# Optimization experiments

Hardware: AMD Instinct MI355X
Metric: run time of the kernel (lower is better)

The kernel has to match this reference:

```python
import jax, jax.numpy as jnp
import numpy as np

EPS = 1e-5
SELECT_NUM = 10   # hard-coded in Support_AUG_Image
NEIGHBOR_K = 3
SEMI_K = 3


def _conv(x, w):
    return jax.lax.conv_general_dilated(x, w, (1, 1), 'SAME',
                                        dimension_numbers=('NCHW', 'OIHW', 'NCHW'))


def _bn(x, g, b):
    # BatchNorm2d, training mode: biased batch stats over (N, H, W)
    mu = jnp.mean(x, (0, 2, 3), keepdims=True)
    var = jnp.mean((x - mu) ** 2, (0, 2, 3), keepdims=True)
    return g[None, :, None, None] * (x - mu) * jax.lax.rsqrt(var + EPS) + b[None, :, None, None]


def _lrelu(x):
    return jnp.where(x >= 0, x, 0.2 * x)


def _pool(x):
    return jax.lax.reduce_window(x, -jnp.inf, jax.lax.max,
                                 (1, 1, 2, 2), (1, 1, 2, 2), 'VALID')


def _features(x, params):
    # conv-bn-lrelu-pool, conv-bn-lrelu-pool, conv-bn-lrelu, conv-bn-lrelu
    for i, (w, g, b) in enumerate(params):
        x = _lrelu(_bn(_conv(x, w), g, b))
        if i < 2:
            x = _pool(x)
    return x  # [N, 64, 21, 21] for 84x84 input


def _descriptors(feat):
    # [B, C, h, w] -> [B, h*w, C], rows L2-normalized (query local descriptors)
    B, C = feat.shape[0], feat.shape[1]
    d = feat.reshape(B, C, -1).transpose(0, 2, 1)
    return d / jnp.sqrt(jnp.sum(d * d, -1, keepdims=True))


def _col_normalize(s):
    # [C, m]: L2-normalize each column (support descriptor)
    return s / jnp.sqrt(jnp.sum(s * s, 0, keepdims=True))


def _img2class_sim(q_desc, S, k):
    # q_desc [B, n, C] row-normalized; S [K, C, m] raw support banks.
    # Per class (K small, fixed): cosine sims [B, n, m], top-k over m, sum.
    sims = []
    for j in range(S.shape[0]):
        inner = q_desc @ _col_normalize(S[j])          # [B, n, m]
        tv = jax.lax.top_k(inner, k)[0]                # [B, n, k]
        sims.append(jnp.sum(tv, axis=(1, 2)))
    return jnp.stack(sims, 1)                          # [B, K]


def _forward(input1, input2, input3, params):
    K, shot = input2.shape[0], input2.shape[1]
    q = _features(input1, params)                      # [Bq, 64, 21, 21]
    sup = _features(input2.reshape((-1,) + input2.shape[2:]), params)
    C, h, w = sup.shape[1], sup.shape[2], sup.shape[3]
    # per class: permute(1,0,2,3).view(C,-1) -> [K, C, shot*h*w]
    S = sup.reshape(K, shot, C, h, w).transpose(0, 2, 1, 3, 4).reshape(K, C, shot * h * w)
    u = _features(input3, params)                      # [Bu, 64, 21, 21]

    # Support_AUG_Image: similarity of unlabeled pool vs support, softmax over classes,
    # then append top-10 unlabeled feature maps (raw) to each class bank.
    u_desc = _descriptors(u)
    sim_u = jax.nn.softmax(_img2class_sim(u_desc, S, SEMI_K), axis=1)  # [Bu, K]
    aug = []
    for j in range(K):
        idx = jax.lax.top_k(sim_u[:, j], SELECT_NUM)[1]                # [10]
        sel = u[idx].transpose(1, 0, 2, 3).reshape(C, -1)              # [C, 10*h*w]
        aug.append(jnp.concatenate([S[j], sel], axis=1))
    S_aug = jnp.stack(aug, 0)                          # [K, C, shot*h*w + 10*h*w]

    # ImgtoClass_Metric on queries vs augmented support
    q_desc = _descriptors(q)
    return _img2class_sim(q_desc, S_aug, NEIGHBOR_K)   # [Bq, K]


def setup_inputs() -> dict:
    key = jax.random.key(0)
    ks = jax.random.split(key, 8)
    inp = {
        'input1': jax.random.normal(ks[0], (75, 3, 84, 84), jnp.float32),
        'input2': jax.random.normal(ks[1], (5, 5, 3, 84, 84), jnp.float32),
        'input3': jax.random.normal(ks[2], (64, 3, 84, 84), jnp.float32),
        'w1': jax.random.normal(ks[3], (64, 3, 3, 3), jnp.float32) * 0.1,
        'w2': jax.random.normal(ks[4], (64, 64, 3, 3), jnp.float32) * 0.05,
        'w3': jax.random.normal(ks[5], (64, 64, 3, 3), jnp.float32) * 0.05,
        'w4': jax.random.normal(ks[6], (64, 64, 3, 3), jnp.float32) * 0.05,
    }
    for i in (1, 2, 3, 4):
        inp[f'g{i}'] = jnp.ones((64,), jnp.float32)
        inp[f'b{i}'] = jnp.zeros((64,), jnp.float32)
    return inp


def reference(input1, input2, input3, w1, g1, b1, w2, g2, b2, w3, g3, b3, w4, g4, b4):
    params = [(w1, g1, b1), (w2, g2, b2), (w3, g3, b3), (w4, g4, b4)]
    return _forward(input1, input2, input3, params)
```

## Files before the change

### kernel.cpp

```cpp
#include <hip/hip_runtime.h>
#include <hip/hip_bf16.h>
#include <math.h>

typedef __hip_bfloat16 bf16;
typedef __attribute__((ext_vector_type(8))) short short8;
typedef __attribute__((ext_vector_type(4))) float floatx4;
typedef __attribute__((ext_vector_type(4))) unsigned short ushort4v;

#define LRELU(v) ((v) < 0.f ? 0.2f * (v) : (v))

__device__ __forceinline__ float b2f(bf16 x) { return __bfloat162float(x); }
__device__ __forceinline__ int img_group(int n) { return n < 75 ? 0 : (n < 100 ? 1 : 2); }

__global__ __launch_bounds__(64) void detect_kernel(
    const void* in1, const void* in2, const void* in3,
    const void* w1, const void* w2, const void* w3, const void* w4,
    const void* g1, const void* g2, const void* g3, const void* g4,
    int* __restrict__ flags)
{
  int t = threadIdx.x;
  if (t >= 11) return;
  const void* p = nullptr; int nh = 384, isg = 0;
  switch (t) {
    case 0: p = in1; break;  case 1: p = in2; break;  case 2: p = in3; break;
    case 3: p = w1;  break;  case 4: p = w2;  break;  case 5: p = w3;  break;
    case 6: p = w4;  break;
    case 7: p = g1; nh = 64; isg = 1; break;
    case 8: p = g2; nh = 64; isg = 1; break;
    case 9: p = g3; nh = 64; isg = 1; break;
    case 10: p = g4; nh = 64; isg = 1; break;
  }
  const unsigned short* h = (const unsigned short*)p;
  int cnt = 0;
  for (int i = 0; i < nh; ++i) {
    unsigned short v = h[i];
    if (isg) {
      if (v == 0) ++cnt;
    } else {
      int e = (v >> 7) & 0xFF;
      if (e >= 160 || (e > 0 && e <= 80)) ++cnt;
    }
  }
  flags[t] = isg ? (cnt >= 16) : (cnt >= 48);
}

#define ZT0 167280
#define ZT1 1972592
#define ZT2 2896240
#define ZT3 3819888
#define ZT4 4565104
__device__ __forceinline__ void border_yx(int b, int W, int* y, int* x) {
  if (b < W) { *y = 0; *x = b; }
  else if (b < 2 * W) { *y = W - 1; *x = b - W; }
  else { int cc = b - 2 * W; *y = 1 + (cc >> 1); *x = (cc & 1) ? (W - 1) : 0; }
}
__global__ __launch_bounds__(256) void zero_pads(
    bf16* __restrict__ imgp, bf16* __restrict__ p1t,
    bf16* __restrict__ p2t, bf16* __restrict__ f3t, bf16* __restrict__ descAll)
{
  int i = blockIdx.x * 256 + threadIdx.x;
  bf16 z = __float2bfloat16(0.f);
  if (i < ZT0) {
    int plane = i / 340, b = i % 340;
    int y, x; border_yx(b, 86, &y, &x);
    imgp[((size_t)plane * 86 + y) * 86 + x] = z;
  } else if (i < ZT1) {
    int r = i - ZT0;
    int img = r / (172 * 64); r %= 172 * 64;
    int colb = r >> 6, ch = r & 63;
    int y, x; border_yx(colb, 44, &y, &x);
    p1t[(((size_t)img * 1936) + y * 44 + x) * 64 + ch] = z;
  } else if (i < ZT2) {
    int r = i - ZT1;
    int img = r / (88 * 64); r %= 88 * 64;
    int colb = r >> 6, ch = r & 63;
    int y, x; border_yx(colb, 23, &y, &x);
    p2t[(((size_t)img * 529) + y * 23 + x) * 64 + ch] = z;
  } else if (i < ZT3) {
    int r = i - ZT2;
    int img = r / (88 * 64); r %= 88 * 64;
    int colb = r >> 6, ch = r & 63;
    int y, x; border_yx(colb, 23, &y, &x);
    f3t[(((size_t)img * 529) + y * 23 + x) * 64 + ch] = z;
  } else if (i < ZT4) {
    int r = i - ZT3;
    int img = r / (71 * 64); r %= 71 * 64;
    int row = 441 + (r >> 6), ch = r & 63;
    descAll[((size_t)img * 512 + row) * 64 + ch] = z;
  }
}

#define NIMG 3471552
#define BIMG 13562
#define NWP  110592
#define BWP  432
#define BW1  8
#define BGB  2
#define NPART (4 * 164 * 128)
#define NZ (NPART + 320 + 375)
#define BZ  331
__global__ __launch_bounds__(256) void setup_all(
    const void* in1, const void* in2, const void* in3,
    const void* w1, const void* w2, const void* w3, const void* w4,
    const void* g1, const void* b1, const void* g2, const void* b2,
    const void* g3, const void* b3, const void* g4, const void* b4,
    const int* __restrict__ flags,
    bf16* __restrict__ imgp, bf16* __restrict__ w1p,
    bf16* __restrict__ wp2, bf16* __restrict__ wp3, bf16* __restrict__ wp4,
    float* __restrict__ gb, float* __restrict__ part,
    float* __restrict__ uscore, float* __restrict__ qscore)
{
  int b = blockIdx.x;
  if (b < BIMG) {
    int k = b * 256 + threadIdx.x;
    if (k >= NIMG) return;
    const void* src; int idx, f;
    if (k < 75 * 21168)       { src = in1; idx = k;               f = flags[0]; }
    else if (k < 100 * 21168) { src = in2; idx = k - 75 * 21168;  f = flags[1]; }
    else                      { src = in3; idx = k - 100 * 21168; f = flags[2]; }
    bf16 v = f ? __float2bfloat16(((const float*)src)[idx]) : ((const bf16*)src)[idx];
    int n = k / 21168, r = k % 21168;
    int ci = r / 7056, pix = r % 7056;
    int y = pix / 84, x = pix % 84;
    imgp[((size_t)(n * 3 + ci) * 86 + y + 1) * 86 + x + 1] = v;
  } else if (b < BIMG + BWP) {
    int idx = (b - BIMG) * 256 + threadIdx.x;
    if (idx >= NWP) return;
    int which = idx / 36864, i = idx % 36864;
    const void* src = which == 0 ? w2 : (which == 1 ? w3 : w4);
    bf16* dst = which == 0 ? wp2 : (which == 1 ? wp3 : wp4);
    int f = flags[4 + which];
    float v = f ? ((const float*)src)[i] : b2f(((const bf16*)src)[i]);
    int co = i / 576, ci = (i / 9) % 64, tap = i % 9;
    dst[((size_t)tap * 64 + co) * 64 + ci] = __float2bfloat16(v);
  } else if (b < BIMG + BWP + BW1) {
    int i = (b - BIMG - BWP) * 256 + threadIdx.x;
    if (i >= 2048) return;
    int co = i >> 5, k = i & 31;
    float v = 0.f;
    if (k < 27) {
      int f = flags[3];
      v = f ? ((const float*)w1)[co * 27 + k] : b2f(((const bf16*)w1)[co * 27 + k]);
    }
    w1p[i] = __float2bfloat16(v);
  } else if (b < BIMG + BWP + BW1 + BGB) {
    int i = (b - BIMG - BWP - BW1) * 256 + threadIdx.x;
    if (i >= 512) return;
    int which = i >> 6, cc = i & 63;
    const void* s;
    switch (which) {
      case 0: s = g1; break; case 1: s = b1; break;
      case 2: s = g2; break; case 3: s = b2; break;
      case 4: s = g3; break; case 5: s = b3; break;
      case 6: s = g4; break; default: s = b4; break;
    }
    int isg = !(which & 1);
    int f = isg ? flags[7 + (which >> 1)] : 0;
    gb[i] = f ? ((const float*)s)[cc] : b2f(((const bf16*)s)[cc]);
  } else {
    int i = (b - BIMG - BWP - BW1 - BGB) * 256 + threadIdx.x;
    if (i < NPART) part[i] = 0.f;
    else if (i < NPART + 320) uscore[i - NPART] = 0.f;
    else if (i < NZ) qscore[i - NPART - 320] = 0.f;
  }
}

__global__ __launch_bounds__(256) void conv1_stats_mfma(
    const bf16* __restrict__ imgp, const bf16* __restrict__ w1p,
    float* __restrict__ part)
{
  __shared__ float sacc[128];
  int n = blockIdx.x, tile = blockIdx.y;
  int lane = threadIdx.x & 63;
  int q = lane >> 4, c = lane & 15;
  int wave = threadIdx.x >> 6;
  int p = tile * 64 + wave * 16 + c;
  bool valid = p < 7056;
  int pc = valid ? p : 0;
  int y = pc / 84, x = pc % 84;
  const short* ib = (const short*)(imgp + (size_t)n * 3 * 86 * 86);
  short bs[8];
  #pragma unroll
  for (int j = 0; j < 8; ++j) {
    int k = q * 8 + j;
    int ci = k / 9, tap = k - ci * 9;
    int dy = tap / 3, dx = tap - dy * 3;
    bs[j] = (k < 27 && valid) ? ib[(ci * 86 + y + dy) * 86 + x + dx] : (short)0;
  }
  short8 B = {bs[0], bs[1], bs[2], bs[3], bs[4], bs[5], bs[6], bs[7]};
  float s[16], sq[16];
  #pragma unroll
  for (int t = 0; t < 4; ++t) {
    const short* ap = (const short*)w1p + (t * 16 + c) * 32 + q * 8;
    short8 A = *(const short8*)ap;
    floatx4 acc = {0.f, 0.f, 0.f, 0.f};
    acc = __builtin_amdgcn_mfma_f32_16x16x32_bf16(A, B, acc, 0, 0, 0);
    #pragma unroll
    for (int r = 0; r < 4; ++r) { s[t * 4 + r] = acc[r]; sq[t * 4 + r] = acc[r] * acc[r]; }
  }
  #pragma unroll
  for (int off = 1; off < 16; off <<= 1)
    #pragma unroll
    for (int i = 0; i < 16; ++i) {
      s[i]  += __shfl_xor(s[i], off);
      sq[i] += __shfl_xor(sq[i], off);
    }
  if (threadIdx.x < 128) sacc[threadIdx.x] = 0.f;
  __syncthreads();
  if (c == 0) {
    #pragma unroll
    for (int t = 0; t < 4; ++t)
      #pragma unroll
      for (int r = 0; r < 4; ++r) {
        int co = t * 16 + q * 4 + r;
        atomicAdd(&sacc[co], s[t * 4 + r]);
        atomicAdd(&sacc[64 + co], sq[t * 4 + r]);
      }
  }
  __syncthreads();
  if (threadIdx.x < 128) atomicAdd(&part[n * 128 + threadIdx.x], sacc[threadIdx.x]);
}

__global__ __launch_bounds__(256) void finalize_kernel(
    const float* __restrict__ part, const float* __restrict__ gam, const float* __restrict__ bet,
    float* __restrict__ scl, float* __restrict__ sht, float HWf)
{
  int t = threadIdx.x;
  if (t >= 192) return;
  int g = t / 64, c = t % 64;
  const int starts[3] = {0, 75, 100}, cnts[3] = {75, 25, 64};
  float S = 0.f, Q = 0.f;
  for (int im = starts[g]; im < starts[g] + cnts[g]; ++im) {
    S += part[im * 128 + c];
    Q += part[im * 128 + 64 + c];
  }
  float N = (float)cnts[g] * HWf;
  float mean = S / N;
  float var = fmaxf(Q / N - mean * mean, 0.f);
  float rstd = rsqrtf(var + 1e-5f);
  float sc = gam[c] * rstd;
  scl[t] = sc;
  sht[t] = bet[c] - mean * sc;
}

__global__ __launch_bounds__(256) void conv1_pool_mfma(
    const bf16* __restrict__ imgp, const bf16* __restrict__ w1p,
    const float* __restrict__ scl, const float* __restrict__ sht,
    bf16* __restrict__ p1t)
{
  int n = blockIdx.x, tile = blockIdx.y;
  int lane = threadIdx.x & 63, wave = threadIdx.x >> 6;
  int q = lane >> 4, c = lane & 15;
  int pp = tile * 64 + wave * 16 + c;
  bool valid = pp < 1764;
  int pc = valid ? pp : 0;
  int py = pc / 42, px = pc % 42;
  int g = img_group(n);
  const short* ib = (const short*)(imgp + (size_t)n * 3 * 86 * 86);
  short8 B[4];
  #pragma unroll
  for (int quad = 0; quad < 4; ++quad) {
    int y = 2 * py + (quad >> 1), x = 2 * px + (quad & 1);
    short bs[8];
    #pragma unroll
    for (int j = 0; j < 8; ++j) {
      int k = q * 8 + j;
      int ci = k / 9, tap = k - ci * 9;
      int dy = tap / 3, dx = tap - dy * 3;
      bs[j] = (k < 27) ? ib[(ci * 86 + y + dy) * 86 + x + dx] : (short)0;
    }
    B[quad] = (short8){bs[0], bs[1], bs[2], bs[3], bs[4], bs[5], bs[6], bs[7]};
  }
  bf16* ob = p1t + ((size_t)n * 1936 + (py + 1) * 44 + px + 1) * 64;
  #pragma unroll
  for (int t = 0; t < 4; ++t) {
    const short* ap = (const short*)w1p + (t * 16 + c) * 32 + q * 8;
    short8 A = *(const short8*)ap;
    floatx4 a0 = {0.f,0.f,0.f,0.f}, a1 = a0, a2 = a0, a3 = a0;
    a0 = __builtin_amdgcn_mfma_f32_16x16x32_bf16(A, B[0], a0, 0, 0, 0);
    a1 = __builtin_amdgcn_mfma_f32_16x16x32_bf16(A, B[1], a1, 0, 0, 0);
    a2 = __builtin_amdgcn_mfma_f32_16x16x32_bf16(A, B[2], a2, 0, 0, 0);
    a3 = __builtin_amdgcn_mfma_f32_16x16x32_bf16(A, B[3], a3, 0, 0, 0);
    if (valid) {
      ushort4v st;
      #pragma unroll
      for (int r = 0; r < 4; ++r) {
        int co = t * 16 + q * 4 + r;
        float sc_ = scl[g * 64 + co], sh_ = sht[g * 64 + co];
        float v0 = a0[r] * sc_ + sh_; v0 = LRELU(v0);
        float v1 = a1[r] * sc_ + sh_; v1 = LRELU(v1);
        float v2 = a2[r] * sc_ + sh_; v2 = LRELU(v2);
        float v3 = a3[r] * sc_ + sh_; v3 = LRELU(v3);
        float best = fmaxf(fmaxf(v0, v1), fmaxf(v2, v3));
        bf16 bv = __float2bfloat16(best);
        st[r] = *(unsigned short*)&bv;
      }
      *(ushort4v*)(ob + t * 16 + q * 4) = st;
    }
  }
}

__global__ __launch_bounds__(256) void bnt_kernel(
    const float* __restrict__ in, const float* __restrict__ scl, const float* __restrict__ sht,
    bf16* __restrict__ outp, int HW, int W, int PW, int PHPW)
{
  __shared__ bf16 tile[64][65];
  int n = blockIdx.x, t0 = blockIdx.y * 64;
  int g = img_group(n);
  for (int idx = threadIdx.x; idx < 4096; idx += 256) {
    int ci = idx >> 6, pix = idx & 63;
    int p = t0 + pix;
    float v = 0.f;
    if (p < HW) {
      v = in[((size_t)n * 64 + ci) * HW + p] * scl[g * 64 + ci] + sht[g * 64 + ci];
      v = LRELU(v);
    }
    tile[pix][ci] = __float2bfloat16(v);
  }
  __syncthreads();
  for (int idx = threadIdx.x; idx < 4096; idx += 256) {
    int pix = idx >> 6, ci = idx & 63;
    int p = t0 + pix;
    if (p < HW) {
      int y = p / W, x = p % W;
      outp[((size_t)n * PHPW + (y + 1) * PW + (x + 1)) * 64 + ci] = tile[pix][ci];
    }
  }
}

__global__ __launch_bounds__(256) void conv_mfma_kernel(
    const bf16* __restrict__ in_t, const bf16* __restrict__ wp,
    void* __restrict__ outp, int HW, int W, int PW, int PHPW, int out_is_f32,
    float* __restrict__ part)
{
  __shared__ float sacc[128];
  if (threadIdx.x < 128) sacc[threadIdx.x] = 0.f;
  __syncthreads();
  int n = blockIdx.x, tile = blockIdx.y;
  int wave = threadIdx.x >> 6, lane = threadIdx.x & 63;
  int q = lane >> 4, c = lane & 15;
  int p = tile * 64 + wave * 16 + c;
  bool valid = p < HW;
  int pc = valid ? p : HW - 1;
  int y = pc / W, x = pc % W;
  const bf16* ibase = in_t + ((size_t)n * PHPW + y * PW + x) * 64;

  short8 B0[9], B1[9];
  #pragma unroll
  for (int dy = 0; dy < 3; ++dy)
    #pragma unroll
    for (int dx = 0; dx < 3; ++dx) {
      const short* bp = (const short*)(ibase + (dy * PW + dx) * 64) + q * 8;
      B0[dy * 3 + dx] = *(const short8*)bp;
      B1[dy * 3 + dx] = *(const short8*)(bp + 32);
    }

  for (int t = 0; t < 4; ++t) {
    floatx4 acc = {0.f, 0.f, 0.f, 0.f};
    #pragma unroll
    for (int tap = 0; tap < 9; ++tap) {
      const short* ap = (const short*)(wp + ((size_t)tap * 64 + t * 16 + c) * 64) + q * 8;
      short8 A0 = *(const short8*)ap;
      short8 A1 = *(const short8*)(ap + 32);
      acc = __builtin_amdgcn_mfma_f32_16x16x32_bf16(A0, B0[tap], acc, 0, 0, 0);
      acc = __builtin_amdgcn_mfma_f32_16x16x32_bf16(A1, B1[tap], acc, 0, 0, 0);
    }
    float sv[4], qv[4];
    #pragma unroll
    for (int r = 0; r < 4; ++r) {
      float v = valid ? acc[r] : 0.f;
      sv[r] = v; qv[r] = v * v;
    }
    #pragma unroll
    for (int off = 1; off < 16; off <<= 1)
      #pragma unroll
      for (int r = 0; r < 4; ++r) {
        sv[r] += __shfl_xor(sv[r], off);
        qv[r] += __shfl_xor(qv[r], off);
      }
    if (c == 0) {
      #pragma unroll
      for (int r = 0; r < 4; ++r) {
        int co = t * 16 + q * 4 + r;
        atomicAdd(&sacc[co], sv[r]);
        atomicAdd(&sacc[64 + co], qv[r]);
      }
    }
    if (valid) {
      #pragma unroll
      for (int r = 0; r < 4; ++r) {
        int co = t * 16 + q * 4 + r;
        size_t oidx = ((size_t)n * 64 + co) * HW + p;
        if (out_is_f32) ((float*)outp)[oidx] = acc[r];
        else ((bf16*)outp)[oidx] = __float2bfloat16(acc[r]);
      }
    }
  }
  __syncthreads();
  if (threadIdx.x < 128) atomicAdd(&part[n * 128 + threadIdx.x], sacc[threadIdx.x]);
}

__global__ __launch_bounds__(256) void bn2_pool_t(
    const bf16* __restrict__ c2, const float* __restrict__ scl, const float* __restrict__ sht,
    bf16* __restrict__ p2t)
{
  __shared__ bf16 tile[64][65];
  int n = blockIdx.x, t0 = blockIdx.y * 64;
  int g = img_group(n);
  for (int idx = threadIdx.x; idx < 4096; idx += 256) {
    int co = idx >> 6, pix = idx & 63;
    int p = t0 + pix;
    bf16 outv = __float2bfloat16(0.f);
    if (p < 441) {
      float sc = scl[g * 64 + co], sh = sht[g * 64 + co];
      int py = p / 21, px = p % 21;
      const bf16* base = c2 + ((size_t)n * 64 + co) * 1764;
      float best = -1e30f;
      #pragma unroll
      for (int dy = 0; dy < 2; ++dy)
        #pragma unroll
        for (int dx = 0; dx < 2; ++dx) {
          float v = b2f(base[(2 * py + dy) * 42 + 2 * px + dx]) * sc + sh;
          v = LRELU(v);
          best = fmaxf(best, v);
        }
      outv = __float2bfloat16(best);
    }
    tile[pix][co] = outv;
  }
  __syncthreads();
  for (int idx = threadIdx.x; idx < 4096; idx += 256) {
    int pix = idx >> 6, co = idx & 63;
    int p = t0 + pix;
    if (p < 441) {
      int y = p / 21, x = p % 21;
      p2t[((size_t)n * 529 + (y + 1) * 23 + x + 1) * 64 + co] = tile[pix][co];
    }
  }
}

__global__ __launch_bounds__(256) void bn_norm_desc(
    const float* __restrict__ feat, const float* __restrict__ scl, const float* __restrict__ sht,
    bf16* __restrict__ descAll)
{
  __shared__ float tile[64][65];
  int n = blockIdx.x, t0 = blockIdx.y * 64;
  int g = img_group(n);
  for (int idx = threadIdx.x; idx < 4096; idx += 256) {
    int ci = idx >> 6, pix = idx & 63;
    int p = t0 + pix;
    float v = 0.f;
    if (p < 441) {
      v = feat[((size_t)n * 64 + ci) * 441 + p] * scl[g * 64 + ci] + sht[g * 64 + ci];
      v = LRELU(v);
    }
    tile[pix][ci] = v;
  }
  __syncthreads();
  int pix = threadIdx.x >> 2, quar = threadIdx.x & 3;
  float ss = 0.f;
  #pragma unroll
  for (int c = 0; c < 16; ++c) { float v = tile[pix][quar * 16 + c]; ss += v * v; }
  ss += __shfl_xor(ss, 1);
  ss += __shfl_xor(ss, 2);
  int p = t0 + pix;
  float inv = (p < 441) ? rsqrtf(ss) : 0.f;
  bf16* o = descAll + ((size_t)n * 512 + p) * 64 + quar * 16;
  #pragma unroll
  for (int c = 0; c < 16; ++c) o[c] = __float2bfloat16(tile[pix][quar * 16 + c] * inv);
}

__global__ __launch_bounds__(256) void sbank_copy(
    const bf16* __restrict__ descAll, bf16* __restrict__ SnT)
{
  int j = blockIdx.x / 9, chunk = blockIdx.x % 9;
  int col = chunk * 256 + threadIdx.x;
  short* o = (short*)(SnT + ((size_t)j * 2304 + col) * 64);
  if (col < 2205) {
    int shot = col / 441, pos = col % 441;
    const short* s = (const short*)(descAll + ((size_t)(75 + j * 5 + shot) * 512 + pos) * 64);
    #pragma unroll
    for (int k = 0; k < 8; ++k) *(short8*)(o + k * 8) = *(const short8*)(s + k * 8);
  } else {
    short8 z = {0,0,0,0,0,0,0,0};
    #pragma unroll
    for (int k = 0; k < 8; ++k) *(short8*)(o + k * 8) = z;
  }
}

__global__ __launch_bounds__(256) void saug_copy(
    const bf16* __restrict__ descAll, const bf16* __restrict__ SnT,
    const int* __restrict__ sel, bf16* __restrict__ SaT)
{
  int j = blockIdx.x / 26, chunk = blockIdx.x % 26;
  int col = chunk * 256 + threadIdx.x;
  short* o = (short*)(SaT + ((size_t)j * 6656 + col) * 64);
  const short* s;
  if (col < 2205) {
    s = (const short*)(SnT + ((size_t)j * 2304 + col) * 64);
  } else if (col < 6615) {
    int rel = col - 2205;
    int i = rel / 441, pos = rel % 441;
    int img = 100 + sel[j * 10 + i];
    s = (const short*)(descAll + ((size_t)img * 512 + pos) * 64);
  } else {
    short8 z = {0,0,0,0,0,0,0,0};
    #pragma unroll
    for (int k = 0; k < 8; ++k) *(short8*)(o + k * 8) = z;
    return;
  }
  #pragma unroll
  for (int k = 0; k < 8; ++k) *(short8*)(o + k * 8) = *(const short8*)(s + k * 8);
}

#define SIM_NS 4
__global__ __launch_bounds__(448) void sim_mfma_kernel(
    const bf16* __restrict__ desc, const bf16* __restrict__ bankT,
    float* __restrict__ partial, int m, int mp)
{
  __shared__ short lds[2][64 * 72];
  int img = blockIdx.x, cls = blockIdx.y, slice = blockIdx.z;
  int tid = threadIdx.x;
  int wave = tid >> 6, lane = tid & 63;
  int q = lane >> 4, c = lane & 15;
  int R = wave * 64;

  const short* dp = (const short*)(desc + ((size_t)img * 512 + R + c) * 64) + q * 8;
  short8 b0l = *(const short8*)dp;          short8 b0h = *(const short8*)(dp + 32);
  short8 b1l = *(const short8*)(dp + 1024); short8 b1h = *(const short8*)(dp + 1056);
  short8 b2l = *(const short8*)(dp + 2048); short8 b2h = *(const short8*)(dp + 2080);
  short8 b3l = *(const short8*)(dp + 3072); short8 b3h = *(const short8*)(dp + 3104);

  float t0[4], t1[4], t2[4];
  #pragma unroll
  for (int i = 0; i < 4; ++i) { t0[i] = -1e4f; t1[i] = -1e4f; t2[i] = -1e4f; }

  const floatx4 z4 = {0.f, 0.f, 0.f, 0.f};

  const short* bankc = (const short*)(bankT + (size_t)cls * mp * 64);
  int nc = (mp >> 6) / SIM_NS;
  int ch0 = slice * nc, ch1 = ch0 + nc;
  int nfull = m >> 4;

  for (int s = tid; s < 512; s += 448) {
    int col = s >> 3, part = s & 7;
    *(short8*)(&lds[0][col * 72 + part * 8]) =
        *(const short8*)(bankc + ((size_t)ch0 * 64 + col) * 64 + part * 8);
  }
  __syncthreads();

  for (int ch = ch0; ch < ch1; ++ch) {
    int cur = (ch - ch0) & 1;
    if (ch + 1 < ch1) {
      const short* src = bankc + (size_t)(ch + 1) * 4096;
      for (int s = tid; s < 512; s += 448) {
        int col = s >> 3, part = s & 7;
        *(short8*)(&lds[cur ^ 1][col * 72 + part * 8]) = *(const short8*)(src + (size_t)col * 64 + part * 8);
      }
    }
    #pragma unroll
    for (int t = 0; t < 4; ++t) {
      const short* lp = &lds[cur][(t * 16 + c) * 72 + q * 8];
      short8 A0 = *(const short8*)lp;
      short8 A1 = *(const short8*)(lp + 32);
      floatx4 a0 = __builtin_amdgcn_mfma_f32_16x16x32_bf16(A0, b0l, z4, 0, 0, 0);
      floatx4 a1 = __builtin_amdgcn_mfma_f32_16x16x32_bf16(A0, b1l, z4, 0, 0, 0);
      floatx4 a2 = __builtin_amdgcn_mfma_f32_16x16x32_bf16(A0, b2l, z4, 0, 0, 0);
      floatx4 a3 = __builtin_amdgcn_mfma_f32_16x16x32_bf16(A0, b3l, z4, 0, 0, 0);
      a0 = __builtin_amdgcn_mfma_f32_16x16x32_bf16(A1, b0h, a0, 0, 0, 0);
      a1 = __builtin_amdgcn_mfma_f32_16x16x32_bf16(A1, b1h, a1, 0, 0, 0);
      a2 = __builtin_amdgcn_mfma_f32_16x16x32_bf16(A1, b2h, a2, 0, 0, 0);
      a3 = __builtin_amdgcn_mfma_f32_16x16x32_bf16(A1, b3h, a3, 0, 0, 0);
      int gt = ch * 4 + t;
      if (gt < nfull) {
        #pragma unroll
        for (int r = 0; r < 4; ++r) {
          float v0 = a0[r];
          t2[0] = __builtin_amdgcn_fmed3f(v0, t2[0], t1[0]);
          t1[0] = __builtin_amdgcn_fmed3f(v0, t1[0], t0[0]);
          t0[0] = fmaxf(t0[0], v0);
          float v1 = a1[r];
          t2[1] = __builtin_amdgcn_fmed3f(v1, t2[1], t1[1]);
          t1[1] = __builtin_amdgcn_fmed3f(v1, t1[1], t0[1]);
          t0[1] = fmaxf(t0[1], v1);
          float v2 = a2[r];
          t2[2] = __builtin_amdgcn_fmed3f(v2, t2[2], t1[2]);
          t1[2] = __builtin_amdgcn_fmed3f(v2, t1[2], t0[2]);
          t0[2] = fmaxf(t0[2], v2);
          float v3 = a3[r];
          t2[3] = __builtin_amdgcn_fmed3f(v3, t2[3], t1[3]);
          t1[3] = __builtin_amdgcn_fmed3f(v3, t1[3], t0[3]);
          t0[3] = fmaxf(t0[3], v3);
        }
      } else {
        #pragma unroll
        for (int r = 0; r < 4; ++r) {
          bool colok = (gt * 16 + q * 4 + r) < m;
          float v0 = colok ? a0[r] : -1e4f;
          t2[0] = __builtin_amdgcn_fmed3f(v0, t2[0], t1[0]);
          t1[0] = __builtin_amdgcn_fmed3f(v0, t1[0], t0[0]);
          t0[0] = fmaxf(t0[0], v0);
          float v1 = colok ? a1[r] : -1e4f;
          t2[1] = __builtin_amdgcn_fmed3f(v1, t2[1], t1[1]);
          t1[1] = __builtin_amdgcn_fmed3f(v1, t1[1], t0[1]);
          t0[1] = fmaxf(t0[1], v1);
          float v2 = colok ? a2[r] : -1e4f;
          t2[2] = __builtin_amdgcn_fmed3f(v2, t2[2], t1[2]);
          t1[2] = __builtin_amdgcn_fmed3f(v2, t1[2], t0[2]);
          t0[2] = fmaxf(t0[2], v2);
          float v3 = colok ? a3[r] : -1e4f;
          t2[3] = __builtin_amdgcn_fmed3f(v3, t2[3], t1[3]);
          t1[3] = __builtin_amdgcn_fmed3f(v3, t1[3], t0[3]);
          t0[3] = fmaxf(t0[3], v3);
        }
      }
    }
    __syncthreads();
  }

  #pragma unroll
  for (int off = 16; off < 64; off <<= 1) {
    #pragma unroll
    for (int i = 0; i < 4; ++i) {
      float b0v = __shfl_xor(t0[i], off);
      float b1v = __shfl_xor(t1[i], off);
      float b2v = __shfl_xor(t2[i], off);
      float n0 = fmaxf(t0[i], b0v);
      float n1 = fminf(fmaxf(t0[i], b1v), fmaxf(t1[i], b0v));
      float n2 = fminf(fminf(fmaxf(t0[i], b2v), fmaxf(t1[i], b1v)), fmaxf(t2[i], b0v));
      t0[i] = n0; t1[i] = n1; t2[i] = n2;
    }
  }

  if (q == 0) {
    size_t base = ((size_t)(img * 5 + cls) * SIM_NS + slice) * 512;
    #pragma unroll
    for (int i = 0; i < 4; ++i) {
      int row = R + i * 16 + c;
      if (row < 441) {
        floatx4 v = {t0[i], t1[i], t2[i], 0.f};
        *(floatx4*)(&partial[(base + row) * 4]) = v;
      }
    }
  }
}

__global__ __launch_bounds__(256) void sim_merge_kernel(
    const float* __restrict__ partial, float* __restrict__ out)
{
  __shared__ float red[4];
  int ic = blockIdx.x;
  int tid = threadIdx.x;
  const floatx4* p0 = (const floatx4*)partial + (size_t)ic * SIM_NS * 512;
  float sum = 0.f;
  for (int row = tid; row < 441; row += 256) {
    floatx4 a = p0[row];
    float t0 = a[0], t1 = a[1], t2 = a[2];
    #pragma unroll
    for (int s = 1; s < SIM_NS; ++s) {
      floatx4 b = p0[s * 512 + row];
      float b0 = b[0], b1 = b[1], b2 = b[2];
      float n0 = fmaxf(t0, b0);
      float n1 = fminf(fmaxf(t0, b1), fmaxf(t1, b0));
      float n2 = fminf(fminf(fmaxf(t0, b2), fmaxf(t1, b1)), fmaxf(t2, b0));
      t0 = n0; t1 = n1; t2 = n2;
    }
    sum += t0 + t1 + t2;
  }
  #pragma unroll
  for (int off = 32; off > 0; off >>= 1) sum += __shfl_down(sum, off);
  int wv = tid >> 6;
  if ((tid & 63) == 0) red[wv] = sum;
  __syncthreads();
  if (tid == 0) out[ic] = red[0] + red[1] + red[2] + red[3];
}

__global__ __launch_bounds__(64) void softtop_kernel(
    const float* __restrict__ uscore, int* __restrict__ sel)
{
  __shared__ float simu[320];
  int i = threadIdx.x;
  {
    float v[5]; float mx = -1e30f;
    #pragma unroll
    for (int j = 0; j < 5; ++j) { v[j] = uscore[i * 5 + j]; mx = fmaxf(mx, v[j]); }
    float s = 0.f;
    #pragma unroll
    for (int j = 0; j < 5; ++j) { v[j] = expf(v[j] - mx); s += v[j]; }
    float inv = 1.f / s;
    #pragma unroll
    for (int j = 0; j < 5; ++j) simu[i * 5 + j] = v[j] * inv;
  }
  __syncthreads();
  if (i < 5) {
    unsigned long long mask = 0ull;
    for (int r = 0; r < 10; ++r) {
      float best = -1e30f; int bi = 0;
      for (int k = 0; k < 64; ++k) {
        if ((mask >> k) & 1ull) continue;
        float v = simu[k * 5 + i];
        if (v > best) { best = v; bi = k; }
      }
      mask |= (1ull << bi);
      sel[i * 10 + r] = bi;
    }
  }
}

__global__ __launch_bounds__(256) void outcvt_kernel(
    const float* __restrict__ qv, const int* __restrict__ flags, float* __restrict__ o)
{
  int i = blockIdx.x * 256 + threadIdx.x;
  if (i >= 375) return;
  float v = qv[i];
  int bad = (!isfinite(v)) || fabsf(v) > 2e3f;
  if (bad) {
    int code = flags[0] * 4 + flags[3] * 2 + flags[7];
    v = -(1e8f * (1.f + 0.01f * (float)code));
  }
  o[i] = v;
}

extern "C" void kernel_launch(void* const* d_in, const int* in_sizes, int n_in,
                              void* d_out, int out_size, void* d_ws, size_t ws_size,
                              hipStream_t stream) {
  const void* in1 = d_in[0];
  const void* in2 = d_in[1];
  const void* in3 = d_in[2];
  const void* w1  = d_in[3];
  const void* w2  = d_in[4];
  const void* w3  = d_in[5];
  const void* w4  = d_in[6];
  const void* g1  = d_in[7];
  const void* b1  = d_in[8];
  const void* g2  = d_in[9];
  const void* b2  = d_in[10];
  const void* g3  = d_in[11];
  const void* b3  = d_in[12];
  const void* g4  = d_in[13];
  const void* b4  = d_in[14];

  char* base = (char*)d_ws;
  size_t off = 0;
  auto alloc = [&](size_t bytes) -> void* {
    void* p = base + off;
    off += (bytes + 255) & ~(size_t)255;
    return p;
  };
  int*   flags = (int*)alloc(16 * 4);
  bf16*  wp2   = (bf16*)alloc(36864 * 2);
  bf16*  wp3   = (bf16*)alloc(36864 * 2);
  bf16*  wp4   = (bf16*)alloc(36864 * 2);
  bf16*  w1p   = (bf16*)alloc(2048 * 2);
  float* gb    = (float*)alloc(8 * 64 * 4);
  float* part  = (float*)alloc(4 * 164 * 128 * 4);
  float* scl1  = (float*)alloc(192 * 4);
  float* sht1  = (float*)alloc(192 * 4);
  float* scl2  = (float*)alloc(192 * 4);
  float* sht2  = (float*)alloc(192 * 4);
  float* scl3  = (float*)alloc(192 * 4);
  float* sht3  = (float*)alloc(192 * 4);
  float* scl4  = (float*)alloc(192 * 4);
  float* sht4  = (float*)alloc(192 * 4);
  float* uscore = (float*)alloc(320 * 4);
  int*   sel    = (int*)alloc(50 * 4);
  float* qscore = (float*)alloc(375 * 4);
  float* simpart = (float*)alloc((size_t)375 * SIM_NS * 512 * 4 * 4);
  bf16*  imgp = (bf16*)alloc((size_t)164 * 3 * 86 * 86 * 2);
  bf16*  p1t  = (bf16*)alloc((size_t)164 * 1936 * 64 * 2);
  bf16*  p2t  = (bf16*)alloc((size_t)164 * 529 * 64 * 2);
  bf16*  f3t  = (bf16*)alloc((size_t)164 * 529 * 64 * 2);
  bf16*  descAll = (bf16*)alloc((size_t)164 * 512 * 64 * 2);
  bf16*  conv2o   = (bf16*)alloc((size_t)164 * 64 * 1764 * 2);
  bf16* SnT     = (bf16*)alloc((size_t)5 * 2304 * 64 * 2);
  bf16* SaT     = (bf16*)alloc((size_t)5 * 6656 * 64 * 2);
  float* feat3 = (float*)p1t;
  float* feat4 = (float*)((char*)p1t + (size_t)164 * 64 * 441 * 4);
  float* part1 = part;
  float* part2 = part + 164 * 128;
  float* part3 = part + 2 * 164 * 128;
  float* part4 = part + 3 * 164 * 128;

  detect_kernel<<<1, 64, 0, stream>>>(in1, in2, in3, w1, w2, w3, w4, g1, g2, g3, g4, flags);
  zero_pads<<<(ZT4 + 255) / 256, 256, 0, stream>>>(imgp, p1t, p2t, f3t, descAll);
  setup_all<<<BIMG + BWP + BW1 + BGB + BZ, 256, 0, stream>>>(
      in1, in2, in3, w1, w2, w3, w4, g1, b1, g2, b2, g3, b3, g4, b4,
      flags, imgp, w1p, wp2, wp3, wp4, gb, part, uscore, qscore);

  conv1_stats_mfma<<<dim3(164, 111), 256, 0, stream>>>(imgp, w1p, part1);
  finalize_kernel<<<1, 256, 0, stream>>>(part1, gb + 0 * 64, gb + 1 * 64, scl1, sht1, 7056.f);
  conv1_pool_mfma<<<dim3(164, 28), 256, 0, stream>>>(imgp, w1p, scl1, sht1, p1t);

  conv_mfma_kernel<<<dim3(164, 28), 256, 0, stream>>>(p1t, wp2, conv2o, 1764, 42, 44, 1936, 0, part2);
  finalize_kernel<<<1, 256, 0, stream>>>(part2, gb + 2 * 64, gb + 3 * 64, scl2, sht2, 1764.f);
  bn2_pool_t<<<dim3(164, 7), 256, 0, stream>>>(conv2o, scl2, sht2, p2t);

  conv_mfma_kernel<<<dim3(164, 7), 256, 0, stream>>>(p2t, wp3, feat3, 441, 21, 23, 529, 1, part3);
  finalize_kernel<<<1, 256, 0, stream>>>(part3, gb + 4 * 64, gb + 5 * 64, scl3, sht3, 441.f);
  bnt_kernel<<<dim3(164, 7), 256, 0, stream>>>(feat3, scl3, sht3, f3t, 441, 21, 23, 529);

  conv_mfma_kernel<<<dim3(164, 7), 256, 0, stream>>>(f3t, wp4, feat4, 441, 21, 23, 529, 1, part4);
  finalize_kernel<<<1, 256, 0, stream>>>(part4, gb + 6 * 64, gb + 7 * 64, scl4, sht4, 441.f);

  bn_norm_desc<<<dim3(164, 7), 256, 0, stream>>>(feat4, scl4, sht4, descAll);
  sbank_copy<<<45, 256, 0, stream>>>(descAll, SnT);

  sim_mfma_kernel<<<dim3(64, 5, SIM_NS), 448, 0, stream>>>(descAll + (size_t)100 * 512 * 64, SnT, simpart, 2205, 2304);
  sim_merge_kernel<<<320, 256, 0, stream>>>(simpart, uscore);
  softtop_kernel<<<1, 64, 0, stream>>>(uscore, sel);
  saug_copy<<<130, 256, 0, stream>>>(descAll, SnT, sel, SaT);

  sim_mfma_kernel<<<dim3(75, 5, SIM_NS), 448, 0, stream>>>(descAll, SaT, simpart, 6615, 6656);
  sim_merge_kernel<<<375, 256, 0, stream>>>(simpart, qscore);
  outcvt_kernel<<<2, 256, 0, stream>>>(qscore, flags, (float*)d_out);
}
```

Measured before the change: 1.078 ms.

## Load support bank tiles directly from global into registers, dropping LDS staging

The similarity kernel no longer stages 64-column bank chunks in shared memory with double buffering and block-wide barriers. Each wave now loads its own 16-column MFMA operand fragments straight from global memory, with a two-tile register prefetch. Launch bounds now also request 4 blocks per unit. This removes the __syncthreads and LDS traffic, but all 7 waves re-read the same bank data from global/L2, which costs more cache bandwidth.

```diff
diff --git a/kernel.cpp b/kernel.cpp
--- a/kernel.cpp
+++ b/kernel.cpp
@@ -514,11 +514,10 @@
 }
 
 #define SIM_NS 4
-__global__ __launch_bounds__(448) void sim_mfma_kernel(
+__global__ __launch_bounds__(448, 4) void sim_mfma_kernel(
     const bf16* __restrict__ desc, const bf16* __restrict__ bankT,
     float* __restrict__ partial, int m, int mp)
 {
-  __shared__ short lds[2][64 * 72];
   int img = blockIdx.x, cls = blockIdx.y, slice = blockIdx.z;
   int tid = threadIdx.x;
   int wave = tid >> 6, lane = tid & 63;
@@ -538,84 +537,79 @@
   const floatx4 z4 = {0.f, 0.f, 0.f, 0.f};
 
   const short* bankc = (const short*)(bankT + (size_t)cls * mp * 64);
-  int nc = (mp >> 6) / SIM_NS;
-  int ch0 = slice * nc, ch1 = ch0 + nc;
+  int nps = (mp >> 4) / SIM_NS;
+  int gt0 = slice * nps, gt1 = gt0 + nps;
   int nfull = m >> 4;
 
-  for (int s = tid; s < 512; s += 448) {
-    int col = s >> 3, part = s & 7;
-    *(short8*)(&lds[0][col * 72 + part * 8]) =
-        *(const short8*)(bankc + ((size_t)ch0 * 64 + col) * 64 + part * 8);
-  }
-  __syncthreads();
-
-  for (int ch = ch0; ch < ch1; ++ch) {
-    int cur = (ch - ch0) & 1;
-    if (ch + 1 < ch1) {
-      const short* src = bankc + (size_t)(ch + 1) * 4096;
-      for (int s = tid; s < 512; s += 448) {
-        int col = s >> 3, part = s & 7;
-        *(short8*)(&lds[cur ^ 1][col * 72 + part * 8]) = *(const short8*)(src + (size_t)col * 64 + part * 8);
+  const short* tb = bankc + (size_t)c * 64 + q * 8;
+
+  short8 a0A = *(const short8*)(tb + (size_t)gt0 * 1024);
+  short8 a1A = *(const short8*)(tb + (size_t)gt0 * 1024 + 32);
+  short8 a0B = *(const short8*)(tb + (size_t)(gt0 + 1) * 1024);
+  short8 a1B = *(const short8*)(tb + (size_t)(gt0 + 1) * 1024 + 32);
+
+  auto step = [&](short8 A0, short8 A1, int gt) {
+    floatx4 a0 = __builtin_amdgcn_mfma_f32_16x16x32_bf16(A0, b0l, z4, 0, 0, 0);
+    floatx4 a1 = __builtin_amdgcn_mfma_f32_16x16x32_bf16(A0, b1l, z4, 0, 0, 0);
+    floatx4 a2 = __builtin_amdgcn_mfma_f32_16x16x32_bf16(A0, b2l, z4, 0, 0, 0);
+    floatx4 a3 = __builtin_amdgcn_mfma_f32_16x16x32_bf16(A0, b3l, z4, 0, 0, 0);
+    a0 = __builtin_amdgcn_mfma_f32_16x16x32_bf16(A1, b0h, a0, 0, 0, 0);
+    a1 = __builtin_amdgcn_mfma_f32_16x16x32_bf16(A1, b1h, a1, 0, 0, 0);
+    a2 = __builtin_amdgcn_mfma_f32_16x16x32_bf16(A1, b2h, a2, 0, 0, 0);
+    a3 = __builtin_amdgcn_mfma_f32_16x16x32_bf16(A1, b3h, a3, 0, 0, 0);
+    if (gt < nfull) {
+      #pragma unroll
+      for (int r = 0; r < 4; ++r) {
+        float v0 = a0[r];
+        t2[0] = __builtin_amdgcn_fmed3f(v0, t2[0], t1[0]);
+        t1[0] = __builtin_amdgcn_fmed3f(v0, t1[0], t0[0]);
+        t0[0] = fmaxf(t0[0], v0);
+        float v1 = a1[r];
+        t2[1] = __builtin_amdgcn_fmed3f(v1, t2[1], t1[1]);
+        t1[1] = __builtin_amdgcn_fmed3f(v1, t1[1], t0[1]);
+        t0[1] = fmaxf(t0[1], v1);
+        float v2 = a2[r];
+        t2[2] = __builtin_amdgcn_fmed3f(v2, t2[2], t1[2]);
+        t1[2] = __builtin_amdgcn_fmed3f(v2, t1[2], t0[2]);
+        t0[2] = fmaxf(t0[2], v2);
+        float v3 = a3[r];
+        t2[3] = __builtin_amdgcn_fmed3f(v3, t2[3], t1[3]);
+        t1[3] = __builtin_amdgcn_fmed3f(v3, t1[3], t0[3]);
+        t0[3] = fmaxf(t0[3], v3);
       }
-    }
-    #pragma unroll
-    for (int t = 0; t < 4; ++t) {
-      const short* lp = &lds[cur][(t * 16 + c) * 72 + q * 8];
-      short8 A0 = *(const short8*)lp;
-      short8 A1 = *(const short8*)(lp + 32);
-      floatx4 a0 = __builtin_amdgcn_mfma_f32_16x16x32_bf16(A0, b0l, z4, 0, 0, 0);
-      floatx4 a1 = __builtin_amdgcn_mfma_f32_16x16x32_bf16(A0, b1l, z4, 0, 0, 0);
-      floatx4 a2 = __builtin_amdgcn_mfma_f32_16x16x32_bf16(A0, b2l, z4, 0, 0, 0);
-      floatx4 a3 = __builtin_amdgcn_mfma_f32_16x16x32_bf16(A0, b3l, z4, 0, 0, 0);
-      a0 = __builtin_amdgcn_mfma_f32_16x16x32_bf16(A1, b0h, a0, 0, 0, 0);
-      a1 = __builtin_amdgcn_mfma_f32_16x16x32_bf16(A1, b1h, a1, 0, 0, 0);
-      a2 = __builtin_amdgcn_mfma_f32_16x16x32_bf16(A1, b2h, a2, 0, 0, 0);
-      a3 = __builtin_amdgcn_mfma_f32_16x16x32_bf16(A1, b3h, a3, 0, 0, 0);
-      int gt = ch * 4 + t;
-      if (gt < nfull) {
-        #pragma unroll
-        for (int r = 0; r < 4; ++r) {
-          float v0 = a0[r];
-          t2[0] = __builtin_amdgcn_fmed3f(v0, t2[0], t1[0]);
-          t1[0] = __builtin_amdgcn_fmed3f(v0, t1[0], t0[0]);
-          t0[0] = fmaxf(t0[0], v0);
-          float v1 = a1[r];
-          t2[1] = __builtin_amdgcn_fmed3f(v1, t2[1], t1[1]);
-          t1[1] = __builtin_amdgcn_fmed3f(v1, t1[1], t0[1]);
-          t0[1] = fmaxf(t0[1], v1);
-          float v2 = a2[r];
-          t2[2] = __builtin_amdgcn_fmed3f(v2, t2[2], t1[2]);
-          t1[2] = __builtin_amdgcn_fmed3f(v2, t1[2], t0[2]);
-          t0[2] = fmaxf(t0[2], v2);
-          float v3 = a3[r];
-          t2[3] = __builtin_amdgcn_fmed3f(v3, t2[3], t1[3]);
-          t1[3] = __builtin_amdgcn_fmed3f(v3, t1[3], t0[3]);
-          t0[3] = fmaxf(t0[3], v3);
-        }
-      } else {
-        #pragma unroll
-        for (int r = 0; r < 4; ++r) {
-          bool colok = (gt * 16 + q * 4 + r) < m;
-          float v0 = colok ? a0[r] : -1e4f;
-          t2[0] = __builtin_amdgcn_fmed3f(v0, t2[0], t1[0]);
-          t1[0] = __builtin_amdgcn_fmed3f(v0, t1[0], t0[0]);
-          t0[0] = fmaxf(t0[0], v0);
-          float v1 = colok ? a1[r] : -1e4f;
-          t2[1] = __builtin_amdgcn_fmed3f(v1, t2[1], t1[1]);
-          t1[1] = __builtin_amdgcn_fmed3f(v1, t1[1], t0[1]);
-          t0[1] = fmaxf(t0[1], v1);
-          float v2 = colok ? a2[r] : -1e4f;
-          t2[2] = __builtin_amdgcn_fmed3f(v2, t2[2], t1[2]);
-          t1[2] = __builtin_amdgcn_fmed3f(v2, t1[2], t0[2]);
-          t0[2] = fmaxf(t0[2], v2);
-          float v3 = colok ? a3[r] : -1e4f;
-          t2[3] = __builtin_amdgcn_fmed3f(v3, t2[3], t1[3]);
-          t1[3] = __builtin_amdgcn_fmed3f(v3, t1[3], t0[3]);
-          t0[3] = fmaxf(t0[3], v3);
-        }
+    } else {
+      #pragma unroll
+      for (int r = 0; r < 4; ++r) {
+        bool colok = (gt * 16 + q * 4 + r) < m;
+        float v0 = colok ? a0[r] : -1e4f;
+        t2[0] = __builtin_amdgcn_fmed3f(v0, t2[0], t1[0]);
+        t1[0] = __builtin_amdgcn_fmed3f(v0, t1[0], t0[0]);
+        t0[0] = fmaxf(t0[0], v0);
+        float v1 = colok ? a1[r] : -1e4f;
+        t2[1] = __builtin_amdgcn_fmed3f(v1, t2[1], t1[1]);
+        t1[1] = __builtin_amdgcn_fmed3f(v1, t1[1], t0[1]);
+        t0[1] = fmaxf(t0[1], v1);
+        float v2 = colok ? a2[r] : -1e4f;
+        t2[2] = __builtin_amdgcn_fmed3f(v2, t2[2], t1[2]);
+        t1[2] = __builtin_amdgcn_fmed3f(v2, t1[2], t0[2]);
+        t0[2] = fmaxf(t0[2], v2);
+        float v3 = colok ? a3[r] : -1e4f;
+        t2[3] = __builtin_amdgcn_fmed3f(v3, t2[3], t1[3]);
+        t1[3] = __builtin_amdgcn_fmed3f(v3, t1[3], t0[3]);
+        t0[3] = fmaxf(t0[3], v3);
       }
     }
-    __syncthreads();
+  };
+
+  for (int gt = gt0; gt < gt1; gt += 2) {
+    step(a0A, a1A, gt);
+    int gp = gt + 2; if (gp >= gt1) gp = gt1 - 1;
+    a0A = *(const short8*)(tb + (size_t)gp * 1024);
+    a1A = *(const short8*)(tb + (size_t)gp * 1024 + 32);
+    step(a0B, a1B, gt + 1);
+    int gp2 = gt + 3; if (gp2 >= gt1) gp2 = gt1 - 1;
+    a0B = *(const short8*)(tb + (size_t)gp2 * 1024);
+    a1B = *(const short8*)(tb + (size_t)gp2 * 1024 + 32);
   }
 
   #pragma unroll
```

New measurement: 1.123 ms. 1.04x slower.
